# Kernel optimization log

Measured on AMD Instinct MI355X. Metric: run time of the kernel, lower is better.

The kernel has to match this reference:

```python
import jax, jax.numpy as jnp
import numpy as np

B, C_IN, H, W = 32, 512, 56, 56   # post-backbone feature map (resnet18, chan=64 -> 512 feats)
C_ENC = 64                         # topk_enc_chan
K = 256                            # topk_pxls_nb


def setup_inputs() -> dict:
    key = jax.random.key(0)
    k1, k2, k3 = jax.random.split(key, 3)
    return {
        "features": jax.random.normal(k1, (B, C_IN, H, W), jnp.float32),
        "conv_w": jax.random.normal(k2, (C_ENC, C_IN), jnp.float32) * 0.02,
        "conv_b": jax.random.normal(k3, (C_ENC,), jnp.float32) * 0.02,
    }


def reference(features, conv_w, conv_b):
    # 1x1 conv: [B,C_IN,H,W] -> [B,C_ENC,H,W]
    feats = jnp.einsum('bchw,oc->bohw', features, conv_w) + conv_b[None, :, None, None]
    b, c, h, w = feats.shape
    flat = feats.reshape(b, c, h * w)                      # [B,C,HW]
    # per-pixel squared L2 norm over channels
    norm = jnp.sum(flat * flat, axis=1)                    # [B,HW]
    _, idx = jax.lax.top_k(norm, K)                        # [B,K]
    abs_ = idx % w                                          # x coord
    ord_ = idx // w                                         # y coord
    # gather selected pixel features: mapToList equivalent -> [B,K,C]
    feat_list = jnp.take_along_axis(flat, idx[:, None, :], axis=2).transpose(0, 2, 1)
    x_out = feat_list.mean(axis=1)                         # [B,C]
    # scatter 1s into sparse attention map
    sw = jnp.zeros((b, h * w), feats.dtype).at[jnp.arange(b)[:, None], idx].set(1.0)
    sw = sw.reshape(b, 1, h, w)
    depth = jnp.zeros((b, K, 1), feats.dtype)
    points = jnp.concatenate(
        [abs_[..., None].astype(feats.dtype), ord_[..., None].astype(feats.dtype), depth, feat_list],
        axis=-1)                                           # [B,K,3+C]
    return (x_out, sw, points)
```

## Files before the change

### kernel.cpp

```cpp
#include <hip/hip_runtime.h>

#define B_     32
#define C_IN_  512
#define H_     56
#define W_     56
#define HW_    (H_ * W_)
#define C_ENC_ 64
#define K_     256
#define BHW_   (B_ * HW_)
#define PTS_ROW_ (3 + C_ENC_)

#define CHUNK_ 16
#define NSTEP_ (C_IN_ / CHUNK_)
#define NBUF_  3

__global__ __launch_bounds__(256) void k_transpose_w(
        const float* __restrict__ w, float* __restrict__ wt) {
    int i = blockIdx.x * 256 + threadIdx.x;
    if (i < C_ENC_ * C_IN_) {
        int o = i / C_IN_;
        int c = i % C_IN_;
        wt[c * C_ENC_ + o] = w[i];
    }
}

__device__ __forceinline__ void gload_lds4(const float* g, float* l) {
    __builtin_amdgcn_global_load_lds(
        (const __attribute__((address_space(1))) void*)g,
        (__attribute__((address_space(3))) void*)l, 4, 0, 0);
}

__global__ __launch_bounds__(256) void k_conv_norm(
        const float* __restrict__ F, const float* __restrict__ wt,
        const float* __restrict__ bias, float* __restrict__ norms,
        float* __restrict__ feats) {
    __shared__ float xbuf[NBUF_][CHUNK_][64];
    __shared__ float nrmp[64][4];

    int t = threadIdx.x;
    int pix_l = t & 63;
    int g = __builtin_amdgcn_readfirstlane(t >> 6);
    int pb = blockIdx.x;
    int b = pb / 49;
    int pix0 = (pb % 49) * 64;

    const float* f  = F + (size_t)b * (C_IN_ * HW_) + pix0 + pix_l;
    const float* wg = wt + g * 16;

    float acc[16];
    #pragma unroll
    for (int o = 0; o < 16; ++o) acc[o] = bias[g * 16 + o];

    #pragma unroll
    for (int u = 0; u < 4; ++u)
        gload_lds4(f + (size_t)(g * 4 + u) * HW_, &xbuf[0][g * 4 + u][0]);

    for (int s = 0; s < NSTEP_; ++s) {
        if (s + 1 < NSTEP_) {
            int cn = (s + 1) * CHUNK_ + g * 4;
            int slot = (s + 1) % NBUF_;
            #pragma unroll
            for (int u = 0; u < 4; ++u)
                gload_lds4(f + (size_t)(cn + u) * HW_, &xbuf[slot][g * 4 + u][0]);
            asm volatile("s_waitcnt vmcnt(4)" ::: "memory");
        } else {
            asm volatile("s_waitcnt vmcnt(0)" ::: "memory");
        }
        __builtin_amdgcn_sched_barrier(0);
        __syncthreads();

        int slot = s % NBUF_;
        int cb = s * CHUNK_;
        #pragma unroll
        for (int cl = 0; cl < CHUNK_; ++cl) {
            float x = xbuf[slot][cl][pix_l];
            #pragma unroll
            for (int o = 0; o < 16; ++o)
                acc[o] = fmaf(x, wg[(cb + cl) * C_ENC_ + o], acc[o]);
        }
    }

    #pragma unroll
    for (int o = 0; o < 16; ++o)
        feats[(size_t)(b * C_ENC_ + g * 16 + o) * HW_ + pix0 + pix_l] = acc[o];

    float p = 0.0f;
    #pragma unroll
    for (int o = 0; o < 16; ++o) p = fmaf(acc[o], acc[o], p);
    nrmp[pix_l][g] = p;
    __syncthreads();

    if (t < 64) {
        float nrm = ((nrmp[t][0] + nrmp[t][1]) + nrmp[t][2]) + nrmp[t][3];
        norms[b * HW_ + pix0 + t] = nrm;
    }
}

__global__ __launch_bounds__(512) void k_topk(
        const float* __restrict__ norms, unsigned int* __restrict__ topk,
        float* __restrict__ sw_out) {
    __shared__ unsigned int keys[HW_];
    __shared__ unsigned int hist[256];
    __shared__ unsigned long long sortbuf[512];
    __shared__ unsigned int s_prefix, s_need, s_cnt;
    __shared__ unsigned char flags[HW_];

    int b = blockIdx.x;
    int t = threadIdx.x;
    const float* nb = norms + b * HW_;

    for (int i = t; i < HW_; i += 512) {
        keys[i] = __float_as_uint(nb[i]);
        flags[i] = 0;
    }
    if (t == 0) { s_prefix = 0u; s_need = K_; s_cnt = 0u; }
    for (int i = t; i < 512; i += 512) sortbuf[i] = ~0ULL;

    for (int r = 0; r < 4; ++r) {
        if (t < 256) hist[t] = 0u;
        __syncthreads();
        unsigned int pfx = s_prefix;
        int shift = 24 - 8 * r;
        for (int i = t; i < HW_; i += 512) {
            unsigned int k = keys[i];
            bool ok = (r == 0) || ((k >> (32 - 8 * r)) == pfx);
            if (ok) atomicAdd(&hist[(k >> shift) & 0xFFu], 1u);
        }
        __syncthreads();
        if (t < 64) {
            unsigned int h0 = hist[4 * t + 0];
            unsigned int h1 = hist[4 * t + 1];
            unsigned int h2 = hist[4 * t + 2];
            unsigned int h3 = hist[4 * t + 3];
            unsigned int tot = h0 + h1 + h2 + h3;
            unsigned int suf = tot;
            #pragma unroll
            for (int off = 1; off < 64; off <<= 1) {
                unsigned int v = __shfl_down(suf, off);
                suf += (t + off < 64) ? v : 0u;
            }
            unsigned int g0 = suf;
            unsigned int g1 = suf - h0;
            unsigned int g2 = g1 - h1;
            unsigned int g3 = g2 - h2;
            unsigned int g4 = g3 - h3;
            unsigned int need = s_need;
            if (g0 >= need && g1 < need) { s_prefix = (pfx << 8) | (4u*t+0u); s_need = need - g1; }
            if (g1 >= need && g2 < need) { s_prefix = (pfx << 8) | (4u*t+1u); s_need = need - g2; }
            if (g2 >= need && g3 < need) { s_prefix = (pfx << 8) | (4u*t+2u); s_need = need - g3; }
            if (g3 >= need && g4 < need) { s_prefix = (pfx << 8) | (4u*t+3u); s_need = need - g4; }
        }
        __syncthreads();
    }
    unsigned int T = s_prefix;

    for (int i = t; i < HW_; i += 512) {
        unsigned int k = keys[i];
        if (k >= T) {
            unsigned int pos = atomicAdd(&s_cnt, 1u);
            if (pos < 512)
                sortbuf[pos] = ((unsigned long long)(~k) << 32) | (unsigned int)i;
        }
    }
    __syncthreads();

    for (int kk = 2; kk <= 512; kk <<= 1) {
        for (int j = kk >> 1; j > 0; j >>= 1) {
            int ixj = t ^ j;
            if (ixj > t) {
                unsigned long long a = sortbuf[t], c = sortbuf[ixj];
                bool up = ((t & kk) == 0);
                if ((a > c) == up) { sortbuf[t] = c; sortbuf[ixj] = a; }
            }
            __syncthreads();
        }
    }

    if (t < K_) {
        unsigned long long e = sortbuf[t];
        unsigned int idx = (unsigned int)(e & 0xFFFFFFFFu);
        topk[b * K_ + t] = idx;
        flags[idx] = 1;
    }
    __syncthreads();

    float* swb = sw_out + b * HW_;
    for (int i = t; i < HW_; i += 512)
        swb[i] = flags[i] ? 1.0f : 0.0f;
}

__global__ __launch_bounds__(64) void k_points(
        const float* __restrict__ feats, const unsigned int* __restrict__ topk,
        float* __restrict__ points) {
    int bk = blockIdx.x;
    int b = bk >> 8;
    int o = threadIdx.x;
    unsigned int p = topk[bk];

    float v = feats[(size_t)(b * C_ENC_ + o) * HW_ + p];
    float* row = points + (size_t)bk * PTS_ROW_;
    row[3 + o] = v;
    if (o == 0) {
        row[0] = (float)(p % W_);
        row[1] = (float)(p / W_);
        row[2] = 0.0f;
    }
}

__global__ __launch_bounds__(64) void k_xout(
        const float* __restrict__ feats, const unsigned int* __restrict__ topk,
        float* __restrict__ xout) {
    __shared__ unsigned int sidx[K_];
    int b = blockIdx.x;
    int t = threadIdx.x;
    for (int r = t; r < K_; r += 64) sidx[r] = topk[b * K_ + r];
    __syncthreads();

    const float* fb = feats + (size_t)(b * C_ENC_ + t) * HW_;
    float s = 0.0f;
    #pragma unroll 8
    for (int k = 0; k < K_; ++k) s += fb[sidx[k]];
    xout[b * C_ENC_ + t] = s * (1.0f / K_);
}

extern "C" void kernel_launch(void* const* d_in, const int* in_sizes, int n_in,
                              void* d_out, int out_size, void* d_ws, size_t ws_size,
                              hipStream_t stream) {
    const float* F    = (const float*)d_in[0];
    const float* w    = (const float*)d_in[1];
    const float* bias = (const float*)d_in[2];

    float* out    = (float*)d_out;
    float* xout   = out;
    float* sw     = out + B_ * C_ENC_;
    float* points = sw + BHW_;

    float* feats         = (float*)d_ws;
    float* wt            = feats + (size_t)B_ * C_ENC_ * HW_;
    float* norms         = wt + C_IN_ * C_ENC_;
    unsigned int* topk   = (unsigned int*)(norms + BHW_);

    k_transpose_w<<<128, 256, 0, stream>>>(w, wt);
    k_conv_norm  <<<BHW_ / 64, 256, 0, stream>>>(F, wt, bias, norms, feats);
    k_topk       <<<B_, 512, 0, stream>>>(norms, topk, sw);
    k_points     <<<B_ * K_, 64, 0, stream>>>(feats, topk, points);
    k_xout       <<<B_, 64, 0, stream>>>(feats, topk, xout);
}
```

Before: 163.1 us.

## Use 64-channel double-buffered LDS stages in conv, syncing once per stage

Restructures the conv prefetch pipeline from a 3-deep ring of 16-channel chunks into a double buffer of 64-channel stages, issuing 16 async global-to-LDS loads per wave per stage. The wait and barrier move to the end of each stage, so there are 8 barriers instead of 32 and more loads are in flight during compute. The norm partial buffer is also transposed to avoid LDS bank conflicts. LDS use rises from 12KB to 32KB per block, which may reduce occupancy, and the wait at the end of each stage exposes latency if compute is shorter than the load.

```diff
diff --git a/kernel.cpp b/kernel.cpp
--- a/kernel.cpp
+++ b/kernel.cpp
@@ -10,9 +10,8 @@
 #define BHW_   (B_ * HW_)
 #define PTS_ROW_ (3 + C_ENC_)
 
-#define CHUNK_ 16
-#define NSTEP_ (C_IN_ / CHUNK_)
-#define NBUF_  3
+#define CSTEP_ 64
+#define NSTEP_ (C_IN_ / CSTEP_)
 
 __global__ __launch_bounds__(256) void k_transpose_w(
         const float* __restrict__ w, float* __restrict__ wt) {
@@ -34,8 +33,8 @@
         const float* __restrict__ F, const float* __restrict__ wt,
         const float* __restrict__ bias, float* __restrict__ norms,
         float* __restrict__ feats) {
-    __shared__ float xbuf[NBUF_][CHUNK_][64];
-    __shared__ float nrmp[64][4];
+    __shared__ float xbuf[2][CSTEP_][64];
+    __shared__ float nrmp[4][64];
 
     int t = threadIdx.x;
     int pix_l = t & 63;
@@ -52,32 +51,32 @@
     for (int o = 0; o < 16; ++o) acc[o] = bias[g * 16 + o];
 
     #pragma unroll
-    for (int u = 0; u < 4; ++u)
-        gload_lds4(f + (size_t)(g * 4 + u) * HW_, &xbuf[0][g * 4 + u][0]);
+    for (int u = 0; u < 16; ++u)
+        gload_lds4(f + (size_t)(g * 16 + u) * HW_, &xbuf[0][g * 16 + u][0]);
+    asm volatile("s_waitcnt vmcnt(0)" ::: "memory");
+    __syncthreads();
 
     for (int s = 0; s < NSTEP_; ++s) {
         if (s + 1 < NSTEP_) {
-            int cn = (s + 1) * CHUNK_ + g * 4;
-            int slot = (s + 1) % NBUF_;
+            int cn = (s + 1) * CSTEP_ + g * 16;
+            float* dst = &xbuf[(s + 1) & 1][g * 16][0];
             #pragma unroll
-            for (int u = 0; u < 4; ++u)
-                gload_lds4(f + (size_t)(cn + u) * HW_, &xbuf[slot][g * 4 + u][0]);
-            asm volatile("s_waitcnt vmcnt(4)" ::: "memory");
-        } else {
-            asm volatile("s_waitcnt vmcnt(0)" ::: "memory");
-        }
-        __builtin_amdgcn_sched_barrier(0);
-        __syncthreads();
-
-        int slot = s % NBUF_;
-        int cb = s * CHUNK_;
-        #pragma unroll
-        for (int cl = 0; cl < CHUNK_; ++cl) {
-            float x = xbuf[slot][cl][pix_l];
-            #pragma unroll
-            for (int o = 0; o < 16; ++o)
-                acc[o] = fmaf(x, wg[(cb + cl) * C_ENC_ + o], acc[o]);
-        }
+            for (int u = 0; u < 16; ++u)
+                gload_lds4(f + (size_t)(cn + u) * HW_, dst + u * 64);
+        }
+        {
+            const float* xb = &xbuf[s & 1][0][0];
+            int cb = s * CSTEP_;
+            #pragma unroll 8
+            for (int cl = 0; cl < CSTEP_; ++cl) {
+                float x = xb[cl * 64 + pix_l];
+                #pragma unroll
+                for (int o = 0; o < 16; ++o)
+                    acc[o] = fmaf(x, wg[(cb + cl) * C_ENC_ + o], acc[o]);
+            }
+        }
+        asm volatile("s_waitcnt vmcnt(0)" ::: "memory");
+        __syncthreads();
     }
 
     #pragma unroll
@@ -87,11 +86,11 @@
     float p = 0.0f;
     #pragma unroll
     for (int o = 0; o < 16; ++o) p = fmaf(acc[o], acc[o], p);
-    nrmp[pix_l][g] = p;
+    nrmp[g][pix_l] = p;
     __syncthreads();
 
     if (t < 64) {
-        float nrm = ((nrmp[t][0] + nrmp[t][1]) + nrmp[t][2]) + nrmp[t][3];
+        float nrm = ((nrmp[0][t] + nrmp[1][t]) + nrmp[2][t]) + nrmp[3][t];
         norms[b * HW_ + pix0 + t] = nrm;
     }
 }
```

Measured after the change: 161.7 us. Within noise of the previous version (-0.8%).
